# Optimization experiments

Measured on AMD Instinct MI355X. Metric: run time of the kernel, lower is better.

Reference implementation:

```python
import jax, jax.numpy as jnp
import numpy as np

B, T, D, H = 4, 4096, 1024, 16
HD = D // H
K = 3  # local_kernel
DIL = 1
EPS = 1e-5


def _ln(x, g, b):
    m = x.mean(-1, keepdims=True)
    v = ((x - m) ** 2).mean(-1, keepdims=True)
    return (x - m) * jax.lax.rsqrt(v + EPS) * g + b


def setup_inputs() -> dict:
    key = jax.random.key(0)
    ks = jax.random.split(key, 6)
    s = 0.02
    return {
        "x": jax.random.normal(ks[0], (B, T, D), jnp.float32),
        "ln_g": jnp.ones((D,), jnp.float32),
        "ln_b": jnp.zeros((D,), jnp.float32),
        "w_qkv": (jax.random.normal(ks[1], (3 * D, D), jnp.float32) * s),  # torch Linear weight [out,in]
        "conv_w": (jax.random.normal(ks[2], (D, 1, K), jnp.float32) * s),  # depthwise conv [D,1,K]
        "conv_b": jnp.zeros((D,), jnp.float32),
        "gln_g": jnp.ones((D,), jnp.float32),
        "gln_b": jnp.zeros((D,), jnp.float32),
        "w_gate": (jax.random.normal(ks[3], (D, D), jnp.float32) * s),
        "b_gate": jnp.zeros((D,), jnp.float32),
        "w_out": (jax.random.normal(ks[4], (D, D), jnp.float32) * s),
        "b_out": jnp.zeros((D,), jnp.float32),
    }


def reference(x, ln_g, ln_b, w_qkv, conv_w, conv_b, gln_g, gln_b, w_gate, b_gate, w_out, b_out):
    b, t, d = x.shape
    x_norm = _ln(x, ln_g, ln_b)

    # QKV projection (no bias)
    qkv = x_norm @ w_qkv.T  # [b,t,3d]
    q, k, v = jnp.split(qkv, 3, axis=-1)
    to_heads = lambda z: z.reshape(b, t, H, HD).transpose(0, 2, 1, 3)  # [b,h,t,hd]
    q, k, v = to_heads(q), to_heads(k), to_heads(v)

    # ELU-feature linear attention (no denominator, matching source)
    phi_q = jax.nn.elu(q) + 1.0
    phi_k = jax.nn.elu(k) + 1.0
    kv = jnp.einsum('bhtd,bhte->bhde', phi_k, v)      # [b,h,hd,hd]
    y_att = jnp.einsum('bhtd,bhde->bhte', phi_q, kv)  # [b,h,t,hd]
    y_att = y_att.transpose(0, 2, 1, 3).reshape(b, t, d)

    # Depthwise local conv branch on x_norm
    pad = (K - 1) // 2 * DIL
    y_local = jax.lax.conv_general_dilated(
        x_norm.transpose(0, 2, 1), conv_w,
        window_strides=(1,), padding=[(pad, pad)], rhs_dilation=(DIL,),
        feature_group_count=d, dimension_numbers=('NCH', 'OIH', 'NCH'))
    y_local = (y_local + conv_b[None, :, None]).transpose(0, 2, 1)  # [b,t,d]

    # Gate: LN -> Linear -> Sigmoid on raw x
    g = jax.nn.sigmoid(_ln(x, gln_g, gln_b) @ w_gate.T + b_gate)

    y = g * y_att + (1.0 - g) * y_local
    return x + (y @ w_out.T + b_out)
```

## Files before the change

### kernel.cpp

```cpp
#include <hip/hip_runtime.h>
#include <hip/hip_bf16.h>

#define B_ 4
#define T_ 4096
#define D_ 1024
#define H_ 16
#define M_ (B_*T_)

typedef short bf16x8 __attribute__((ext_vector_type(8)));
typedef float f32x4 __attribute__((ext_vector_type(4)));

__device__ __forceinline__ float b2f(unsigned short h){
  union { unsigned u; float f; } x; x.u = ((unsigned)h) << 16; return x.f;
}
__device__ __forceinline__ unsigned short f2b(float f){
  union { float f; unsigned u; } x; x.f = f;
  unsigned r = x.u + 0x7FFFu + ((x.u >> 16) & 1u);
  return (unsigned short)(r >> 16);
}

__device__ __forceinline__ void ld_lds16(const unsigned short* g, unsigned short* l){
  __builtin_amdgcn_global_load_lds(
      (const __attribute__((address_space(1))) unsigned int*)(unsigned long long)g,
      (__attribute__((address_space(3))) unsigned int*)(unsigned int)(unsigned long long)l,
      16, 0, 0);
}

__global__ __launch_bounds__(256) void f32_to_bf16(const float* __restrict__ src,
                                                   unsigned short* __restrict__ dst, int n){
  int i = (blockIdx.x*256 + threadIdx.x)*4;
  if (i < n){
    float4 v = *(const float4*)(src + i);
    ushort4 o; o.x=f2b(v.x); o.y=f2b(v.y); o.z=f2b(v.z); o.w=f2b(v.w);
    *(ushort4*)(dst + i) = o;
  }
}

__global__ __launch_bounds__(256) void ln_dual(
    const float* __restrict__ x,
    const float* __restrict__ g1, const float* __restrict__ b1,
    const float* __restrict__ g2, const float* __restrict__ b2,
    unsigned short* __restrict__ xn, unsigned short* __restrict__ xg){
  int row = blockIdx.x;
  int tid = threadIdx.x;
  const float4* xr = (const float4*)(x + (size_t)row*D_);
  float4 v = xr[tid];
  float s  = v.x+v.y+v.z+v.w;
  float ss = v.x*v.x + v.y*v.y + v.z*v.z + v.w*v.w;
  #pragma unroll
  for (int o=32;o>0;o>>=1){ s += __shfl_down(s,o,64); ss += __shfl_down(ss,o,64); }
  __shared__ float red[8];
  int lane = tid & 63, wv = tid >> 6;
  if (lane==0){ red[wv]=s; red[4+wv]=ss; }
  __syncthreads();
  s  = red[0]+red[1]+red[2]+red[3];
  ss = red[4]+red[5]+red[6]+red[7];
  float mean = s * (1.f/D_);
  float var  = ss*(1.f/D_) - mean*mean;
  float inv  = rsqrtf(var + 1e-5f);
  int c = tid*4;
  float4 ga = *(const float4*)(g1+c), ba = *(const float4*)(b1+c);
  float4 gb = *(const float4*)(g2+c), bb = *(const float4*)(b2+c);
  float nx=(v.x-mean)*inv, ny=(v.y-mean)*inv, nz=(v.z-mean)*inv, nw=(v.w-mean)*inv;
  size_t base = (size_t)row*D_ + c;
  ushort4 o1, o2;
  o1.x=f2b(nx*ga.x+ba.x); o1.y=f2b(ny*ga.y+ba.y); o1.z=f2b(nz*ga.z+ba.z); o1.w=f2b(nw*ga.w+ba.w);
  o2.x=f2b(nx*gb.x+bb.x); o2.y=f2b(ny*gb.y+bb.y); o2.z=f2b(nz*gb.z+bb.z); o2.w=f2b(nw*gb.w+bb.w);
  *(ushort4*)(xn+base) = o1;
  *(ushort4*)(xg+base) = o2;
}

template<int EPI>
__global__ __launch_bounds__(256, 3) void gemm_bt(
    const unsigned short* __restrict__ A, const unsigned short* __restrict__ Bw,
    int N, int K,
    const float* __restrict__ bias, const float* __restrict__ resid,
    unsigned short* __restrict__ Cb, float* __restrict__ Cf){
  __shared__ unsigned short sA[128*32];
  __shared__ unsigned short sB[128*32];
  int tid = threadIdx.x;
  int lane = tid & 63, wv = tid >> 6;
  int m0 = blockIdx.x * 128, n0 = blockIdx.y * 128;
  int srow = wv*32 + (lane>>2);
  int scol = (lane&3)*8;
  const unsigned short* gA = A + (size_t)(m0+srow)*K + scol;
  const unsigned short* gB = Bw + (size_t)(n0+srow)*K + scol;
  unsigned short* lA = sA + wv*1024;
  unsigned short* lB = sB + wv*1024;
  f32x4 zero = {0.f,0.f,0.f,0.f};
  f32x4 acc[4][4];
  #pragma unroll
  for (int i=0;i<4;i++){ acc[i][0]=zero; acc[i][1]=zero; acc[i][2]=zero; acc[i][3]=zero; }
  int wm = wv & 1, wn = wv >> 1;
  int fr = lane & 15;
  int fk = (lane >> 4) * 8;
  for (int kk = 0; kk < K; kk += 32){
    __syncthreads();
    ld_lds16(gA,              lA);
    ld_lds16(gA + (size_t)16*K, lA + 512);
    ld_lds16(gB,              lB);
    ld_lds16(gB + (size_t)16*K, lB + 512);
    gA += 32; gB += 32;
    __syncthreads();
    bf16x8 af[4], bfr[4];
    #pragma unroll
    for (int i=0;i<4;i++) af[i]  = *(const bf16x8*)(sA + (wm*64 + i*16 + fr)*32 + fk);
    #pragma unroll
    for (int j=0;j<4;j++) bfr[j] = *(const bf16x8*)(sB + (wn*64 + j*16 + fr)*32 + fk);
    #pragma unroll
    for (int i=0;i<4;i++)
      #pragma unroll
      for (int j=0;j<4;j++)
        acc[i][j] = __builtin_amdgcn_mfma_f32_16x16x32_bf16(af[i], bfr[j], acc[i][j], 0,0,0);
  }
  int er = (lane>>4)*4;
  int ec = lane & 15;
  #pragma unroll
  for (int i=0;i<4;i++){
    #pragma unroll
    for (int r=0;r<4;r++){
      int m = m0 + wm*64 + i*16 + er + r;
      size_t rowoff = (size_t)m * N;
      #pragma unroll
      for (int j=0;j<4;j++){
        int n = n0 + wn*64 + j*16 + ec;
        float v = acc[i][j][r];
        if (EPI == 0){
          Cb[rowoff + n] = f2b(v);
        } else if (EPI == 1){
          v += bias[n];
          v = 1.f/(1.f + __expf(-v));
          Cb[rowoff + n] = f2b(v);
        } else {
          v += bias[n] + resid[rowoff + n];
          Cf[rowoff + n] = v;
        }
      }
    }
  }
}

__global__ __launch_bounds__(256) void kv_partial(const unsigned short* __restrict__ qkv,
                                                  float* __restrict__ part){
  int bh = blockIdx.x, chunk = blockIdx.y;
  int b = bh >> 4, h = bh & 15;
  int tid = threadIdx.x;
  int d = tid & 63, wv = tid >> 6;
  __shared__ float sk[512], sv[512];
  float acc[16];
  #pragma unroll
  for (int j=0;j<16;j++) acc[j] = 0.f;
  size_t base = ((size_t)(b*T_) + (size_t)chunk*512) * 3072 + h*64;
  for (int ts=0; ts<512; ts+=8){
    __syncthreads();
    int li = tid & 127;
    int tt = li >> 4;
    int e  = (li & 15) * 4;
    size_t off = base + (size_t)(ts+tt)*3072 + e;
    if (tid < 128){
      ushort4 kr = *(const ushort4*)(qkv + off + 1024);
      float k0=b2f(kr.x), k1=b2f(kr.y), k2=b2f(kr.z), k3=b2f(kr.w);
      float4 ph;
      ph.x = k0>0.f ? k0+1.f : __expf(k0);
      ph.y = k1>0.f ? k1+1.f : __expf(k1);
      ph.z = k2>0.f ? k2+1.f : __expf(k2);
      ph.w = k3>0.f ? k3+1.f : __expf(k3);
      *(float4*)(sk + tt*64 + e) = ph;
    } else {
      ushort4 vr = *(const ushort4*)(qkv + off + 2048);
      float4 vv; vv.x=b2f(vr.x); vv.y=b2f(vr.y); vv.z=b2f(vr.z); vv.w=b2f(vr.w);
      *(float4*)(sv + tt*64 + e) = vv;
    }
    __syncthreads();
    #pragma unroll
    for (int t8=0;t8<8;t8++){
      float pk = sk[t8*64 + d];
      const float4* v4 = (const float4*)(sv + t8*64 + wv*16);
      float4 a0=v4[0], a1=v4[1], a2=v4[2], a3=v4[3];
      acc[0] +=pk*a0.x; acc[1] +=pk*a0.y; acc[2] +=pk*a0.z; acc[3] +=pk*a0.w;
      acc[4] +=pk*a1.x; acc[5] +=pk*a1.y; acc[6] +=pk*a1.z; acc[7] +=pk*a1.w;
      acc[8] +=pk*a2.x; acc[9] +=pk*a2.y; acc[10]+=pk*a2.z; acc[11]+=pk*a2.w;
      acc[12]+=pk*a3.x; acc[13]+=pk*a3.y; acc[14]+=pk*a3.z; acc[15]+=pk*a3.w;
    }
  }
  float* pp = part + (((size_t)chunk*64 + bh)*4096) + d*64 + wv*16;
  #pragma unroll
  for (int j=0;j<16;j++) pp[j] = acc[j];
}

__global__ __launch_bounds__(256) void kv_reduce(const float* __restrict__ part,
                                                 unsigned short* __restrict__ kvb){
  int i = blockIdx.x*256 + threadIdx.x;
  float s = 0.f;
  #pragma unroll
  for (int c=0;c<8;c++) s += part[(size_t)c*262144 + i];
  int bh = i >> 12, de = i & 4095;
  int d = de >> 6, e = de & 63;
  kvb[(bh<<12) + e*64 + d] = f2b(s);
}

__global__ __launch_bounds__(256) void attn_mfma(
    const unsigned short* __restrict__ qkv, const unsigned short* __restrict__ kvb,
    const unsigned short* __restrict__ xn, const unsigned short* __restrict__ gsig,
    const float* __restrict__ conv_w, const float* __restrict__ conv_b,
    unsigned short* __restrict__ y){
  int bh = blockIdx.x;
  int b = bh >> 4, h = bh & 15;
  int t0 = blockIdx.y * 128;
  int tid = threadIdx.x, lane = tid & 63, wv = tid >> 6;
  __shared__ unsigned short sA[128*72];
  __shared__ unsigned short sB[64*72];
  #pragma unroll
  for (int it=0; it<4; it++){
    int idx = it*256 + tid;
    int r = idx >> 3, c = (idx & 7)*8;
    size_t gaddr = ((size_t)(b*T_ + t0 + r))*3072 + h*64 + c;
    bf16x8 u = *(const bf16x8*)(qkv + gaddr);
    bf16x8 o;
    #pragma unroll
    for (int q=0;q<8;q++){
      float f = b2f((unsigned short)u[q]);
      f = f > 0.f ? f + 1.f : __expf(f);
      o[q] = (short)f2b(f);
    }
    *(bf16x8*)(sA + r*72 + c) = o;
  }
  #pragma unroll
  for (int it=0; it<2; it++){
    int idx = it*256 + tid;
    int r = idx >> 3, c = (idx & 7)*8;
    *(bf16x8*)(sB + r*72 + c) = *(const bf16x8*)(kvb + ((size_t)bh<<12) + r*64 + c);
  }
  __syncthreads();
  int fr = lane & 15, fk = (lane >> 4)*8;
  bf16x8 af[2][2], bfr[4][2];
  #pragma unroll
  for (int i=0;i<2;i++)
    #pragma unroll
    for (int ks=0;ks<2;ks++)
      af[i][ks] = *(const bf16x8*)(sA + (wv*32 + i*16 + fr)*72 + ks*32 + fk);
  #pragma unroll
  for (int j=0;j<4;j++)
    #pragma unroll
    for (int ks=0;ks<2;ks++)
      bfr[j][ks] = *(const bf16x8*)(sB + (j*16 + fr)*72 + ks*32 + fk);
  f32x4 zero = {0.f,0.f,0.f,0.f};
  f32x4 acc[2][4];
  #pragma unroll
  for (int i=0;i<2;i++){ acc[i][0]=zero; acc[i][1]=zero; acc[i][2]=zero; acc[i][3]=zero; }
  #pragma unroll
  for (int ks=0;ks<2;ks++)
    #pragma unroll
    for (int i=0;i<2;i++)
      #pragma unroll
      for (int j=0;j<4;j++)
        acc[i][j] = __builtin_amdgcn_mfma_f32_16x16x32_bf16(af[i][ks], bfr[j][ks], acc[i][j], 0,0,0);
  int er = (lane>>4)*4, ec = lane & 15;
  #pragma unroll
  for (int j=0;j<4;j++){
    int d = h*64 + j*16 + ec;
    float w0 = conv_w[d*3], w1 = conv_w[d*3+1], w2 = conv_w[d*3+2], cb = conv_b[d];
    #pragma unroll
    for (int i=0;i<2;i++){
      #pragma unroll
      for (int r=0;r<4;r++){
        int t = t0 + wv*32 + i*16 + er + r;
        size_t base = ((size_t)(b*T_ + t))*1024 + d;
        float ya = acc[i][j][r];
        float xm = (t>0)      ? b2f(xn[base-1024]) : 0.f;
        float xc =              b2f(xn[base]);
        float xp = (t<T_-1)   ? b2f(xn[base+1024]) : 0.f;
        float yl = xm*w0 + xc*w1 + xp*w2 + cb;
        float gg = b2f(gsig[base]);
        y[base] = f2b(gg*ya + (1.f-gg)*yl);
      }
    }
  }
}

extern "C" void kernel_launch(void* const* d_in, const int* in_sizes, int n_in,
                              void* d_out, int out_size, void* d_ws, size_t ws_size,
                              hipStream_t stream){
  const float* x      = (const float*)d_in[0];
  const float* ln_g   = (const float*)d_in[1];
  const float* ln_b   = (const float*)d_in[2];
  const float* w_qkv  = (const float*)d_in[3];
  const float* conv_w = (const float*)d_in[4];
  const float* conv_b = (const float*)d_in[5];
  const float* gln_g  = (const float*)d_in[6];
  const float* gln_b  = (const float*)d_in[7];
  const float* w_gate = (const float*)d_in[8];
  const float* b_gate = (const float*)d_in[9];
  const float* w_out  = (const float*)d_in[10];
  const float* b_out  = (const float*)d_in[11];
  float* out = (float*)d_out;

  char* ws = (char*)d_ws;
  size_t off = 0;
  auto alloc = [&](size_t bytes){ void* p = ws + off; off += (bytes + 255) & ~(size_t)255; return p; };
  unsigned short* wqkv_b  = (unsigned short*)alloc((size_t)3072*1024*2);
  unsigned short* wgate_b = (unsigned short*)alloc((size_t)1024*1024*2);
  unsigned short* wout_b  = (unsigned short*)alloc((size_t)1024*1024*2);
  unsigned short* xn      = (unsigned short*)alloc((size_t)M_*D_*2);
  unsigned short* xg      = (unsigned short*)alloc((size_t)M_*D_*2);
  unsigned short* qkv     = (unsigned short*)alloc((size_t)M_*3072*2);
  unsigned short* gy      = (unsigned short*)alloc((size_t)M_*D_*2);
  float* part             = (float*)alloc((size_t)8*64*4096*4);
  unsigned short* kvb     = (unsigned short*)alloc((size_t)64*4096*2);

  f32_to_bf16<<<3072*1024/1024, 256, 0, stream>>>(w_qkv,  wqkv_b,  3072*1024);
  f32_to_bf16<<<1024*1024/1024, 256, 0, stream>>>(w_gate, wgate_b, 1024*1024);
  f32_to_bf16<<<1024*1024/1024, 256, 0, stream>>>(w_out,  wout_b,  1024*1024);

  ln_dual<<<M_, 256, 0, stream>>>(x, ln_g, ln_b, gln_g, gln_b, xn, xg);

  gemm_bt<0><<<dim3(128,24), 256, 0, stream>>>(xn, wqkv_b, 3072, 1024, nullptr, nullptr, qkv, nullptr);

  kv_partial<<<dim3(64,8), 256, 0, stream>>>(qkv, part);
  kv_reduce<<<1024, 256, 0, stream>>>(part, kvb);

  gemm_bt<1><<<dim3(128,8), 256, 0, stream>>>(xg, wgate_b, 1024, 1024, b_gate, nullptr, gy, nullptr);

  attn_mfma<<<dim3(64,32), 256, 0, stream>>>(qkv, kvb, xn, gy, conv_w, conv_b, gy);

  gemm_bt<2><<<dim3(128,8), 256, 0, stream>>>(gy, wout_b, 1024, 1024, b_out, x, nullptr, out);
}
```

Measured before the change: 498.9 us.

## Swizzle GEMM LDS layout, double KV chunks, and stage attention epilogue through LDS

The GEMM's LDS tiles get an XOR swizzle applied consistently to both the global-to-LDS load column and the fragment read offset, to cut bank conflicts on the MFMA operand reads. The KV partial reduction uses 16 time chunks instead of 8, giving more blocks for the 64 heads at the price of a larger partial buffer and more reduce reads. The attention epilogue now writes accumulators to a shared tile and re-reads them row-wise, so global loads and stores of xn, the gate and y become 16-byte vectorised along channels, and the conv weights are cached in shared memory. The shared tile reuses the operand buffers, so an extra barrier is added before the MFMAs. A no-op ternary appears in one accumulation line.

```diff
diff --git a/kernel.cpp b/kernel.cpp
--- a/kernel.cpp
+++ b/kernel.cpp
@@ -6,6 +6,7 @@
 #define D_ 1024
 #define H_ 16
 #define M_ (B_*T_)
+#define KV_CHUNKS 16
 
 typedef short bf16x8 __attribute__((ext_vector_type(8)));
 typedef float f32x4 __attribute__((ext_vector_type(4)));
@@ -82,7 +83,7 @@
   int lane = tid & 63, wv = tid >> 6;
   int m0 = blockIdx.x * 128, n0 = blockIdx.y * 128;
   int srow = wv*32 + (lane>>2);
-  int scol = (lane&3)*8;
+  int scol = (((lane&3) ^ ((lane>>3)&3)))*8;
   const unsigned short* gA = A + (size_t)(m0+srow)*K + scol;
   const unsigned short* gB = Bw + (size_t)(n0+srow)*K + scol;
   unsigned short* lA = sA + wv*1024;
@@ -93,7 +94,7 @@
   for (int i=0;i<4;i++){ acc[i][0]=zero; acc[i][1]=zero; acc[i][2]=zero; acc[i][3]=zero; }
   int wm = wv & 1, wn = wv >> 1;
   int fr = lane & 15;
-  int fk = (lane >> 4) * 8;
+  int fk = ((lane >> 4) * 8) ^ (((fr>>1)&3)<<3);
   for (int kk = 0; kk < K; kk += 32){
     __syncthreads();
     ld_lds16(gA,              lA);
@@ -150,8 +151,8 @@
   float acc[16];
   #pragma unroll
   for (int j=0;j<16;j++) acc[j] = 0.f;
-  size_t base = ((size_t)(b*T_) + (size_t)chunk*512) * 3072 + h*64;
-  for (int ts=0; ts<512; ts+=8){
+  size_t base = ((size_t)(b*T_) + (size_t)chunk*(T_/KV_CHUNKS)) * 3072 + h*64;
+  for (int ts=0; ts<(T_/KV_CHUNKS); ts+=8){
     __syncthreads();
     int li = tid & 127;
     int tt = li >> 4;
@@ -180,7 +181,7 @@
       acc[0] +=pk*a0.x; acc[1] +=pk*a0.y; acc[2] +=pk*a0.z; acc[3] +=pk*a0.w;
       acc[4] +=pk*a1.x; acc[5] +=pk*a1.y; acc[6] +=pk*a1.z; acc[7] +=pk*a1.w;
       acc[8] +=pk*a2.x; acc[9] +=pk*a2.y; acc[10]+=pk*a2.z; acc[11]+=pk*a2.w;
-      acc[12]+=pk*a3.x; acc[13]+=pk*a3.y; acc[14]+=pk*a3.z; acc[15]+=pk*a3.w;
+      acc[12]+=pk*a3.x; acc[13]+=pk*a3.y; acc[14]+=pk*a3.w==0?pk*a3.z:pk*a3.z; acc[15]+=pk*a3.w;
     }
   }
   float* pp = part + (((size_t)chunk*64 + bh)*4096) + d*64 + wv*16;
@@ -193,7 +194,7 @@
   int i = blockIdx.x*256 + threadIdx.x;
   float s = 0.f;
   #pragma unroll
-  for (int c=0;c<8;c++) s += part[(size_t)c*262144 + i];
+  for (int c=0;c<KV_CHUNKS;c++) s += part[(size_t)c*262144 + i];
   int bh = i >> 12, de = i & 4095;
   int d = de >> 6, e = de & 63;
   kvb[(bh<<12) + e*64 + d] = f2b(s);
@@ -208,8 +209,18 @@
   int b = bh >> 4, h = bh & 15;
   int t0 = blockIdx.y * 128;
   int tid = threadIdx.x, lane = tid & 63, wv = tid >> 6;
-  __shared__ unsigned short sA[128*72];
-  __shared__ unsigned short sB[64*72];
+  __shared__ __align__(16) char smem[128*68*4];
+  unsigned short* sA = (unsigned short*)smem;
+  unsigned short* sB = sA + 128*72;
+  float* sC = (float*)smem;
+  __shared__ float sW[64*4];
+  if (tid < 64){
+    int d = h*64 + tid;
+    sW[tid*4+0] = conv_w[d*3];
+    sW[tid*4+1] = conv_w[d*3+1];
+    sW[tid*4+2] = conv_w[d*3+2];
+    sW[tid*4+3] = conv_b[d];
+  }
   #pragma unroll
   for (int it=0; it<4; it++){
     int idx = it*256 + tid;
@@ -244,6 +255,7 @@
     #pragma unroll
     for (int ks=0;ks<2;ks++)
       bfr[j][ks] = *(const bf16x8*)(sB + (j*16 + fr)*72 + ks*32 + fk);
+  __syncthreads();
   f32x4 zero = {0.f,0.f,0.f,0.f};
   f32x4 acc[2][4];
   #pragma unroll
@@ -257,24 +269,37 @@
         acc[i][j] = __builtin_amdgcn_mfma_f32_16x16x32_bf16(af[i][ks], bfr[j][ks], acc[i][j], 0,0,0);
   int er = (lane>>4)*4, ec = lane & 15;
   #pragma unroll
-  for (int j=0;j<4;j++){
-    int d = h*64 + j*16 + ec;
-    float w0 = conv_w[d*3], w1 = conv_w[d*3+1], w2 = conv_w[d*3+2], cb = conv_b[d];
-    #pragma unroll
-    for (int i=0;i<2;i++){
+  for (int i=0;i<2;i++)
+    #pragma unroll
+    for (int j=0;j<4;j++)
       #pragma unroll
-      for (int r=0;r<4;r++){
-        int t = t0 + wv*32 + i*16 + er + r;
-        size_t base = ((size_t)(b*T_ + t))*1024 + d;
-        float ya = acc[i][j][r];
-        float xm = (t>0)      ? b2f(xn[base-1024]) : 0.f;
-        float xc =              b2f(xn[base]);
-        float xp = (t<T_-1)   ? b2f(xn[base+1024]) : 0.f;
-        float yl = xm*w0 + xc*w1 + xp*w2 + cb;
-        float gg = b2f(gsig[base]);
-        y[base] = f2b(gg*ya + (1.f-gg)*yl);
-      }
-    }
+      for (int r=0;r<4;r++)
+        sC[(wv*32 + i*16 + er + r)*68 + j*16 + ec] = acc[i][j][r];
+  __syncthreads();
+  int row = tid >> 1, cb0 = (tid & 1)*32;
+  int t = t0 + row;
+  size_t gb = ((size_t)(b*T_ + t))*1024 + h*64 + cb0;
+  #pragma unroll
+  for (int c8=0; c8<4; c8++){
+    int cc = cb0 + c8*8;
+    const float4* cp = (const float4*)(sC + row*68 + cc);
+    float4 cv0 = cp[0], cv1 = cp[1];
+    bf16x8 gv = *(const bf16x8*)(gsig + gb + c8*8);
+    bf16x8 xc = *(const bf16x8*)(xn + gb + c8*8);
+    bf16x8 xm = {0,0,0,0,0,0,0,0}, xp = {0,0,0,0,0,0,0,0};
+    if (t > 0)     xm = *(const bf16x8*)(xn + gb + c8*8 - 1024);
+    if (t < T_-1)  xp = *(const bf16x8*)(xn + gb + c8*8 + 1024);
+    bf16x8 o;
+    #pragma unroll
+    for (int q=0;q<8;q++){
+      const float* w = sW + (cc + q)*4;
+      float yl = b2f((unsigned short)xm[q])*w[0] + b2f((unsigned short)xc[q])*w[1]
+               + b2f((unsigned short)xp[q])*w[2] + w[3];
+      float ya = (q < 4) ? ((const float*)&cv0)[q] : ((const float*)&cv1)[q-4];
+      float gg = b2f((unsigned short)gv[q]);
+      o[q] = (short)f2b(gg*ya + (1.f-gg)*yl);
+    }
+    *(bf16x8*)(y + gb + c8*8) = o;
   }
 }
 
@@ -305,7 +330,7 @@
   unsigned short* xg      = (unsigned short*)alloc((size_t)M_*D_*2);
   unsigned short* qkv     = (unsigned short*)alloc((size_t)M_*3072*2);
   unsigned short* gy      = (unsigned short*)alloc((size_t)M_*D_*2);
-  float* part             = (float*)alloc((size_t)8*64*4096*4);
+  float* part             = (float*)alloc((size_t)KV_CHUNKS*64*4096*4);
   unsigned short* kvb     = (unsigned short*)alloc((size_t)64*4096*2);
 
   f32_to_bf16<<<3072*1024/1024, 256, 0, stream>>>(w_qkv,  wqkv_b,  3072*1024);
@@ -316,7 +341,7 @@
 
   gemm_bt<0><<<dim3(128,24), 256, 0, stream>>>(xn, wqkv_b, 3072, 1024, nullptr, nullptr, qkv, nullptr);
 
-  kv_partial<<<dim3(64,8), 256, 0, stream>>>(qkv, part);
+  kv_partial<<<dim3(64,KV_CHUNKS), 256, 0, stream>>>(qkv, part);
   kv_reduce<<<1024, 256, 0, stream>>>(part, kvb);
 
   gemm_bt<1><<<dim3(128,8), 256, 0, stream>>>(xg, wgate_b, 1024, 1024, b_gate, nullptr, gy, nullptr);
```

Result: faster. 473.8 us (-5.0%).
